# Kernel optimization log

Measured on AMD Instinct MI355X. Metric: run time of the kernel, lower is better.

Reference implementation:

```python
import jax, jax.numpy as jnp
import numpy as np

CHUNK = 512
LR = 0.001  # fast-weight learning_rate


def setup_inputs() -> dict:
    key = jax.random.key(0)
    k1, k2, k3, k4 = jax.random.split(key, 4)
    B, S, H, F = 4, 4096, 1024, 4096
    x = jax.random.normal(k1, (B, S, H), dtype=jnp.float32)
    w0 = jax.random.normal(k2, (H, F), dtype=jnp.float32) * 0.02
    w1 = jax.random.normal(k3, (F, H), dtype=jnp.float32) * 0.02
    w2 = jax.random.normal(k4, (H, F), dtype=jnp.float32) * 0.02
    return {"x": x, "w0": w0, "w1": w1, "w2": w2}


def _fast_weight(xc, a0, a1, a2):
    # SwiGLU fast-weight MLP (LaCT-style): [B,C,H] -> [B,C,H]
    h = jax.nn.silu(jnp.einsum('bch,hf->bcf', xc, a0)) * jnp.einsum('bch,hf->bcf', xc, a2)
    return jnp.einsum('bcf,fh->bch', h, a1)


def reference(x, w0, w1, w2):
    B, S, H = x.shape
    nC = S // CHUNK
    # [nC, B, CHUNK, H] so scan iterates over chunks
    xc = x.reshape(B, nC, CHUNK, H).transpose(1, 0, 2, 3)

    def step(carry, x_chunk):
        a0, a1, a2, acc_loss = carry
        out = _fast_weight(x_chunk, a0, a1, a2)
        chunk_loss = jnp.mean((out - x_chunk) ** 2)
        decay = 1.0 - LR * chunk_loss  # per-chunk scalar weight decay
        return (a0 * decay, a1 * decay, a2 * decay, acc_loss + chunk_loss), out

    init = (w0, w1, w2, jnp.float32(0.0))
    (_, _, _, total_loss), outs = jax.lax.scan(step, init, xc)
    output = outs.transpose(1, 0, 2, 3).reshape(B, S, H)
    return output, total_loss / nC
```

## Files before the change

### kernel.cpp

```cpp
#include <hip/hip_runtime.h>

typedef float f32x4 __attribute__((ext_vector_type(4)));
typedef short bf16x8 __attribute__((ext_vector_type(8)));
typedef unsigned short u16;

#define B_SZ 4
#define S_SZ 4096
#define H_SZ 1024
#define F_SZ 4096
#define CHUNK_SZ 512
#define NCHUNK 8
#define MCH 2048
#define LRATE 0.001f
#define NSPLIT 4

__device__ __forceinline__ u16 f2bf(float f) {
  unsigned u = __float_as_uint(f);
  u += 0x7FFFu + ((u >> 16) & 1u);
  return (u16)(u >> 16);
}
__device__ __forceinline__ float bf2f(u16 u) {
  return __uint_as_float(((unsigned)u) << 16);
}

__device__ __forceinline__ void gload_lds16(const void* g, void* l) {
  __builtin_amdgcn_global_load_lds(
      (const __attribute__((address_space(1))) unsigned int*)g,
      (__attribute__((address_space(3))) unsigned int*)l, 16, 0, 0);
}


__global__ __launch_bounds__(256) void k_init(float* scal) {
  if (threadIdx.x == 0) { scal[0] = 1.f; scal[1] = 0.f; }
}

__global__ __launch_bounds__(256) void k_cvt_x(const float* __restrict__ x,
                                               u16* __restrict__ xb) {
  size_t i = ((size_t)blockIdx.x * 256 + threadIdx.x) * 8;
  float4 v0 = *(const float4*)(x + i);
  float4 v1 = *(const float4*)(x + i + 4);
  union { u16 u[8]; bf16x8 v; } o;
  o.u[0] = f2bf(v0.x); o.u[1] = f2bf(v0.y); o.u[2] = f2bf(v0.z); o.u[3] = f2bf(v0.w);
  o.u[4] = f2bf(v1.x); o.u[5] = f2bf(v1.y); o.u[6] = f2bf(v1.z); o.u[7] = f2bf(v1.w);
  *(bf16x8*)(xb + i) = o.v;
}

__global__ __launch_bounds__(256) void k_transpose_cvt(const float* __restrict__ W,
                                                       u16* __restrict__ Wt,
                                                       int R, int C) {
  __shared__ float tile[32][33];
  int tx = threadIdx.x & 31, ty = threadIdx.x >> 5;
  int r0 = blockIdx.y << 5, c0 = blockIdx.x << 5;
#pragma unroll
  for (int i = 0; i < 4; i++)
    tile[ty + i * 8][tx] = W[(size_t)(r0 + ty + i * 8) * C + c0 + tx];
  __syncthreads();
#pragma unroll
  for (int i = 0; i < 4; i++)
    Wt[(size_t)(c0 + ty + i * 8) * R + r0 + tx] = f2bf(tile[tx][ty + i * 8]);
}

__global__ __launch_bounds__(256) void k_gemm_gu(
    const u16* __restrict__ xb,
    const u16* __restrict__ w0t,
    const u16* __restrict__ w2t,
    u16* __restrict__ hbuf,
    const float* __restrict__ scal, int chunk) {
  __shared__ __align__(16) u16 sA[128 * 64];
  __shared__ __align__(16) u16 sB0[64 * 64];
  __shared__ __align__(16) u16 sB2[64 * 64];

  int t = threadIdx.x;
  int lane = t & 63, wid = t >> 6;
  int wm = wid >> 1, wn = wid & 1;
  int tm = blockIdx.x, tn = blockIdx.y;

  int gm0 = tm << 7;
  int bb = gm0 >> 9;
  int pos0 = gm0 & 511;
  const u16* Abase = xb + ((size_t)bb * S_SZ + (size_t)chunk * CHUNK_SZ + pos0) * H_SZ;

  int srow = t >> 3;
  int scol = (((t & 7) ^ (srow & 7)) << 3);
  const u16* aSrc  = Abase + (size_t)srow * H_SZ + scol;
  const u16* b0Src = w0t + ((size_t)(tn << 6) + srow) * H_SZ + scol;
  const u16* b2Src = w2t + ((size_t)(tn << 6) + srow) * H_SZ + scol;
  char* aDst  = (char*)sA  + t * 16;
  char* b0Dst = (char*)sB0 + t * 16;
  char* b2Dst = (char*)sB2 + t * 16;

  f32x4 acc0[4][2], acc2[4][2];
#pragma unroll
  for (int i = 0; i < 4; i++)
#pragma unroll
    for (int j = 0; j < 2; j++)
#pragma unroll
      for (int k = 0; k < 4; k++) { acc0[i][j][k] = 0.f; acc2[i][j][k] = 0.f; }

  int arow = (wm << 6) + (lane & 15);
  int brow = (wn << 5) + (lane & 15);
  int sl0 = (lane >> 4) ^ (lane & 7);
  int sl1 = ((lane >> 4) | 4) ^ (lane & 7);
  const char* aP0 = (const char*)sA + arow * 128 + sl0 * 16;
  const char* aP1 = (const char*)sA + arow * 128 + sl1 * 16;
  const char* b0P0 = (const char*)sB0 + brow * 128 + sl0 * 16;
  const char* b0P1 = (const char*)sB0 + brow * 128 + sl1 * 16;
  const char* b2P0 = (const char*)sB2 + brow * 128 + sl0 * 16;
  const char* b2P1 = (const char*)sB2 + brow * 128 + sl1 * 16;

  for (int k0 = 0; k0 < H_SZ; k0 += 64) {
#pragma unroll
    for (int r = 0; r < 4; r++)
      gload_lds16(aSrc + (size_t)r * 32 * H_SZ, aDst + r * 4096);
#pragma unroll
    for (int r = 0; r < 2; r++) {
      gload_lds16(b0Src + (size_t)r * 32 * H_SZ, b0Dst + r * 4096);
      gload_lds16(b2Src + (size_t)r * 32 * H_SZ, b2Dst + r * 4096);
    }
    aSrc += 64; b0Src += 64; b2Src += 64;
    __syncthreads();

    {
      bf16x8 av[4], b0v[2], b2v[2];
#pragma unroll
      for (int fr = 0; fr < 4; fr++) av[fr] = *(const bf16x8*)(aP0 + fr * 2048);
#pragma unroll
      for (int fc = 0; fc < 2; fc++) {
        b0v[fc] = *(const bf16x8*)(b0P0 + fc * 2048);
        b2v[fc] = *(const bf16x8*)(b2P0 + fc * 2048);
      }
#pragma unroll
      for (int fr = 0; fr < 4; fr++)
#pragma unroll
        for (int fc = 0; fc < 2; fc++) {
          acc0[fr][fc] = __builtin_amdgcn_mfma_f32_16x16x32_bf16(av[fr], b0v[fc], acc0[fr][fc], 0, 0, 0);
          acc2[fr][fc] = __builtin_amdgcn_mfma_f32_16x16x32_bf16(av[fr], b2v[fc], acc2[fr][fc], 0, 0, 0);
        }
    }
    {
      bf16x8 av[4], b0v[2], b2v[2];
#pragma unroll
      for (int fr = 0; fr < 4; fr++) av[fr] = *(const bf16x8*)(aP1 + fr * 2048);
#pragma unroll
      for (int fc = 0; fc < 2; fc++) {
        b0v[fc] = *(const bf16x8*)(b0P1 + fc * 2048);
        b2v[fc] = *(const bf16x8*)(b2P1 + fc * 2048);
      }
#pragma unroll
      for (int fr = 0; fr < 4; fr++)
#pragma unroll
        for (int fc = 0; fc < 2; fc++) {
          acc0[fr][fc] = __builtin_amdgcn_mfma_f32_16x16x32_bf16(av[fr], b0v[fc], acc0[fr][fc], 0, 0, 0);
          acc2[fr][fc] = __builtin_amdgcn_mfma_f32_16x16x32_bf16(av[fr], b2v[fc], acc2[fr][fc], 0, 0, 0);
        }
    }
    __syncthreads();
  }

  float D = scal[0];
#pragma unroll
  for (int fr = 0; fr < 4; fr++)
#pragma unroll
    for (int fc = 0; fc < 2; fc++) {
      int row0 = (tm << 7) + (wm << 6) + (fr << 4) + ((lane >> 4) << 2);
      int col = (tn << 6) + (wn << 5) + (fc << 4) + (lane & 15);
#pragma unroll
      for (int j = 0; j < 4; j++) {
        float g = D * acc0[fr][fc][j];
        float u = D * acc2[fr][fc][j];
        float sil = g / (1.f + __expf(-g));
        hbuf[(size_t)(row0 + j) * F_SZ + col] = f2bf(sil * u);
      }
    }
}

__global__ __launch_bounds__(256) void k_gemm_out(
    const u16* __restrict__ hbuf,
    const u16* __restrict__ w1t,
    u16* __restrict__ pbuf) {
  __shared__ __align__(16) u16 sA[128 * 64];
  __shared__ __align__(16) u16 sB[64 * 64];

  int t = threadIdx.x;
  int lane = t & 63, wid = t >> 6;
  int wm = wid >> 1, wn = wid & 1;
  int tm = blockIdx.x, tn = blockIdx.y, kz = blockIdx.z;

  int srow = t >> 3;
  int scol = (((t & 7) ^ (srow & 7)) << 3);
  const u16* aSrc = hbuf + ((size_t)(tm << 7) + srow) * F_SZ + kz * 1024 + scol;
  const u16* bSrc = w1t + ((size_t)(tn << 6) + srow) * F_SZ + kz * 1024 + scol;
  char* aDst = (char*)sA + t * 16;
  char* bDst = (char*)sB + t * 16;

  f32x4 acc[4][2];
#pragma unroll
  for (int i = 0; i < 4; i++)
#pragma unroll
    for (int j = 0; j < 2; j++)
#pragma unroll
      for (int k = 0; k < 4; k++) acc[i][j][k] = 0.f;

  int arow = (wm << 6) + (lane & 15);
  int brow = (wn << 5) + (lane & 15);
  int sl0 = (lane >> 4) ^ (lane & 7);
  int sl1 = ((lane >> 4) | 4) ^ (lane & 7);
  const char* aP0 = (const char*)sA + arow * 128 + sl0 * 16;
  const char* aP1 = (const char*)sA + arow * 128 + sl1 * 16;
  const char* bP0 = (const char*)sB + brow * 128 + sl0 * 16;
  const char* bP1 = (const char*)sB + brow * 128 + sl1 * 16;

  for (int k0 = 0; k0 < 1024; k0 += 64) {
#pragma unroll
    for (int r = 0; r < 4; r++)
      gload_lds16(aSrc + (size_t)r * 32 * F_SZ, aDst + r * 4096);
#pragma unroll
    for (int r = 0; r < 2; r++)
      gload_lds16(bSrc + (size_t)r * 32 * F_SZ, bDst + r * 4096);
    aSrc += 64; bSrc += 64;
    __syncthreads();

    {
      bf16x8 av[4], bv[2];
#pragma unroll
      for (int fr = 0; fr < 4; fr++) av[fr] = *(const bf16x8*)(aP0 + fr * 2048);
#pragma unroll
      for (int fc = 0; fc < 2; fc++) bv[fc] = *(const bf16x8*)(bP0 + fc * 2048);
#pragma unroll
      for (int fr = 0; fr < 4; fr++)
#pragma unroll
        for (int fc = 0; fc < 2; fc++)
          acc[fr][fc] = __builtin_amdgcn_mfma_f32_16x16x32_bf16(av[fr], bv[fc], acc[fr][fc], 0, 0, 0);
    }
    {
      bf16x8 av[4], bv[2];
#pragma unroll
      for (int fr = 0; fr < 4; fr++) av[fr] = *(const bf16x8*)(aP1 + fr * 2048);
#pragma unroll
      for (int fc = 0; fc < 2; fc++) bv[fc] = *(const bf16x8*)(bP1 + fc * 2048);
#pragma unroll
      for (int fr = 0; fr < 4; fr++)
#pragma unroll
        for (int fc = 0; fc < 2; fc++)
          acc[fr][fc] = __builtin_amdgcn_mfma_f32_16x16x32_bf16(av[fr], bv[fc], acc[fr][fc], 0, 0, 0);
    }
    __syncthreads();
  }

#pragma unroll
  for (int fr = 0; fr < 4; fr++)
#pragma unroll
    for (int fc = 0; fc < 2; fc++) {
      int row0 = (tm << 7) + (wm << 6) + (fr << 4) + ((lane >> 4) << 2);
      int col = (tn << 6) + (wn << 5) + (fc << 4) + (lane & 15);
#pragma unroll
      for (int j = 0; j < 4; j++)
        pbuf[((size_t)kz * MCH + row0 + j) * 1024 + col] = f2bf(acc[fr][fc][j]);
    }
}

__global__ __launch_bounds__(256) void k_epilogue(
    const u16* __restrict__ pbuf, const float* __restrict__ x,
    float* __restrict__ out, const float* __restrict__ scal,
    float* __restrict__ partials, int chunk) {
  __shared__ float red[256];
  int t = threadIdx.x;
  size_t base = ((size_t)blockIdx.x * 256 + t) * 8;
  int row = (int)(base >> 10);
  int col = (int)(base & 1023);
  float D = scal[0];

  float s[8] = {0.f, 0.f, 0.f, 0.f, 0.f, 0.f, 0.f, 0.f};
#pragma unroll
  for (int kz = 0; kz < NSPLIT; kz++) {
    union { bf16x8 v; u16 u[8]; } p;
    p.v = *(const bf16x8*)(pbuf + (size_t)kz * MCH * 1024 + base);
#pragma unroll
    for (int j = 0; j < 8; j++) s[j] += bf2f(p.u[j]);
  }

  int bb = row >> 9, pos = row & 511;
  size_t off = ((size_t)bb * S_SZ + (size_t)chunk * CHUNK_SZ + pos) * H_SZ + col;
  float4 x0 = *(const float4*)(x + off);
  float4 x1 = *(const float4*)(x + off + 4);
  float xv[8] = {x0.x, x0.y, x0.z, x0.w, x1.x, x1.y, x1.z, x1.w};
  float ov[8];
  float psum = 0.f;
#pragma unroll
  for (int j = 0; j < 8; j++) {
    ov[j] = D * s[j];
    float e = ov[j] - xv[j];
    psum += e * e;
  }
  *(float4*)(out + off) = make_float4(ov[0], ov[1], ov[2], ov[3]);
  *(float4*)(out + off + 4) = make_float4(ov[4], ov[5], ov[6], ov[7]);

  red[t] = psum;
  __syncthreads();
  for (int s2 = 128; s2 > 0; s2 >>= 1) {
    if (t < s2) red[t] += red[t + s2];
    __syncthreads();
  }
  if (t == 0) partials[blockIdx.x] = red[0];
}

__global__ __launch_bounds__(256) void k_update(float* scal, const float* __restrict__ partials,
                                                float* lossout, int chunk) {
  __shared__ float red[256];
  int t = threadIdx.x;
  float s = 0.f;
  for (int i = t; i < 1024; i += 256) s += partials[i];
  red[t] = s;
  __syncthreads();
  for (int s2 = 128; s2 > 0; s2 >>= 1) {
    if (t < s2) red[t] += red[t + s2];
    __syncthreads();
  }
  if (t == 0) {
    float loss = red[0] / (float)((size_t)MCH * H_SZ);
    float total = scal[1] + loss;
    scal[1] = total;
    scal[0] = scal[0] * (1.f - LRATE * loss);
    if (chunk == NCHUNK - 1) lossout[0] = total / (float)NCHUNK;
  }
}

extern "C" void kernel_launch(void* const* d_in, const int* in_sizes, int n_in,
                              void* d_out, int out_size, void* d_ws, size_t ws_size,
                              hipStream_t stream) {
  const float* x = (const float*)d_in[0];
  const float* w0 = (const float*)d_in[1];
  const float* w1 = (const float*)d_in[2];
  const float* w2 = (const float*)d_in[3];
  float* out = (float*)d_out;

  char* ws = (char*)d_ws;
  float* scal = (float*)ws;
  float* partials = (float*)(ws + 1024);
  u16* xb = (u16*)(ws + 8192);
  u16* w0t = xb + (size_t)B_SZ * S_SZ * H_SZ;
  u16* w2t = w0t + (size_t)H_SZ * F_SZ;
  u16* w1t = w2t + (size_t)H_SZ * F_SZ;
  u16* hbuf = w1t + (size_t)F_SZ * H_SZ;
  u16* pbuf = hbuf + (size_t)MCH * F_SZ;

  k_init<<<1, 256, 0, stream>>>(scal);
  k_cvt_x<<<(B_SZ * S_SZ * H_SZ) / (256 * 8), 256, 0, stream>>>(x, xb);
  k_transpose_cvt<<<dim3(F_SZ / 32, H_SZ / 32), 256, 0, stream>>>(w0, w0t, H_SZ, F_SZ);
  k_transpose_cvt<<<dim3(H_SZ / 32, F_SZ / 32), 256, 0, stream>>>(w1, w1t, F_SZ, H_SZ);
  k_transpose_cvt<<<dim3(F_SZ / 32, H_SZ / 32), 256, 0, stream>>>(w2, w2t, H_SZ, F_SZ);

  float* lossout = out + (size_t)B_SZ * S_SZ * H_SZ;
  for (int c = 0; c < NCHUNK; c++) {
    k_gemm_gu<<<dim3(16, 64), 256, 0, stream>>>(xb, w0t, w2t, hbuf, scal, c);
    k_gemm_out<<<dim3(16, 16, NSPLIT), 256, 0, stream>>>(hbuf, w1t, pbuf);
    k_epilogue<<<1024, 256, 0, stream>>>(pbuf, x, out, scal, partials, c);
    k_update<<<1, 256, 0, stream>>>(scal, partials, lossout, c);
  }
}
```

Measured before the change: 627.4 us.

## Double-buffer LDS tiles and remap workgroups across XCDs in both GEMMs

Both GEMM kernels now keep two LDS buffers and issue the global-to-LDS loads for the next K step before computing on the current one. This lets memory latency overlap with MFMA work. The workgroup index is also permuted so consecutive blocks land on the same XCD, aiming for better L2 reuse of shared A/B tiles. LDS use doubles, which may lower occupancy, and with a single barrier per iteration the prefetch into the other buffer relies on the previous end-of-loop sync to stay safe.

Result: slower. 700.6 us (+11.7%).

```diff
diff --git a/kernel.cpp b/kernel.cpp
--- a/kernel.cpp
+++ b/kernel.cpp
@@ -66,14 +66,18 @@
     const u16* __restrict__ w2t,
     u16* __restrict__ hbuf,
     const float* __restrict__ scal, int chunk) {
-  __shared__ __align__(16) u16 sA[128 * 64];
-  __shared__ __align__(16) u16 sB0[64 * 64];
-  __shared__ __align__(16) u16 sB2[64 * 64];
+  __shared__ __align__(16) u16 sA[2][128 * 64];
+  __shared__ __align__(16) u16 sB0[2][64 * 64];
+  __shared__ __align__(16) u16 sB2[2][64 * 64];
 
   int t = threadIdx.x;
   int lane = t & 63, wid = t >> 6;
   int wm = wid >> 1, wn = wid & 1;
-  int tm = blockIdx.x, tn = blockIdx.y;
+
+  int orig = blockIdx.x + (gridDim.x * blockIdx.y);
+  int nwg = gridDim.x * gridDim.y;
+  int wg = (orig & 7) * (nwg >> 3) + (orig >> 3);
+  int tm = wg & 15, tn = wg >> 4;
 
   int gm0 = tm << 7;
   int bb = gm0 >> 9;
@@ -101,33 +105,46 @@
   int brow = (wn << 5) + (lane & 15);
   int sl0 = (lane >> 4) ^ (lane & 7);
   int sl1 = ((lane >> 4) | 4) ^ (lane & 7);
-  const char* aP0 = (const char*)sA + arow * 128 + sl0 * 16;
-  const char* aP1 = (const char*)sA + arow * 128 + sl1 * 16;
-  const char* b0P0 = (const char*)sB0 + brow * 128 + sl0 * 16;
-  const char* b0P1 = (const char*)sB0 + brow * 128 + sl1 * 16;
-  const char* b2P0 = (const char*)sB2 + brow * 128 + sl0 * 16;
-  const char* b2P1 = (const char*)sB2 + brow * 128 + sl1 * 16;
-
-  for (int k0 = 0; k0 < H_SZ; k0 += 64) {
-#pragma unroll
-    for (int r = 0; r < 4; r++)
-      gload_lds16(aSrc + (size_t)r * 32 * H_SZ, aDst + r * 4096);
-#pragma unroll
-    for (int r = 0; r < 2; r++) {
-      gload_lds16(b0Src + (size_t)r * 32 * H_SZ, b0Dst + r * 4096);
-      gload_lds16(b2Src + (size_t)r * 32 * H_SZ, b2Dst + r * 4096);
-    }
-    aSrc += 64; b0Src += 64; b2Src += 64;
-    __syncthreads();
-
+  const int aO0 = arow * 128 + sl0 * 16, aO1 = arow * 128 + sl1 * 16;
+  const int bO0 = brow * 128 + sl0 * 16, bO1 = brow * 128 + sl1 * 16;
+
+#pragma unroll
+  for (int r = 0; r < 4; r++)
+    gload_lds16(aSrc + (size_t)r * 32 * H_SZ, aDst + r * 4096);
+#pragma unroll
+  for (int r = 0; r < 2; r++) {
+    gload_lds16(b0Src + (size_t)r * 32 * H_SZ, b0Dst + r * 4096);
+    gload_lds16(b2Src + (size_t)r * 32 * H_SZ, b2Dst + r * 4096);
+  }
+  aSrc += 64; b0Src += 64; b2Src += 64;
+  __syncthreads();
+
+  int cur = 0;
+#pragma unroll 1
+  for (int step = 0; step < H_SZ / 64; step++) {
+    int nxt = cur ^ 1;
+    if (step + 1 < H_SZ / 64) {
+#pragma unroll
+      for (int r = 0; r < 4; r++)
+        gload_lds16(aSrc + (size_t)r * 32 * H_SZ, aDst + nxt * 16384 + r * 4096);
+#pragma unroll
+      for (int r = 0; r < 2; r++) {
+        gload_lds16(b0Src + (size_t)r * 32 * H_SZ, b0Dst + nxt * 8192 + r * 4096);
+        gload_lds16(b2Src + (size_t)r * 32 * H_SZ, b2Dst + nxt * 8192 + r * 4096);
+      }
+      aSrc += 64; b0Src += 64; b2Src += 64;
+    }
+    const char* aB  = (const char*)sA  + cur * 16384;
+    const char* b0B = (const char*)sB0 + cur * 8192;
+    const char* b2B = (const char*)sB2 + cur * 8192;
     {
       bf16x8 av[4], b0v[2], b2v[2];
 #pragma unroll
-      for (int fr = 0; fr < 4; fr++) av[fr] = *(const bf16x8*)(aP0 + fr * 2048);
+      for (int fr = 0; fr < 4; fr++) av[fr] = *(const bf16x8*)(aB + aO0 + fr * 2048);
 #pragma unroll
       for (int fc = 0; fc < 2; fc++) {
-        b0v[fc] = *(const bf16x8*)(b0P0 + fc * 2048);
-        b2v[fc] = *(const bf16x8*)(b2P0 + fc * 2048);
+        b0v[fc] = *(const bf16x8*)(b0B + bO0 + fc * 2048);
+        b2v[fc] = *(const bf16x8*)(b2B + bO0 + fc * 2048);
       }
 #pragma unroll
       for (int fr = 0; fr < 4; fr++)
@@ -140,11 +157,11 @@
     {
       bf16x8 av[4], b0v[2], b2v[2];
 #pragma unroll
-      for (int fr = 0; fr < 4; fr++) av[fr] = *(const bf16x8*)(aP1 + fr * 2048);
+      for (int fr = 0; fr < 4; fr++) av[fr] = *(const bf16x8*)(aB + aO1 + fr * 2048);
 #pragma unroll
       for (int fc = 0; fc < 2; fc++) {
-        b0v[fc] = *(const bf16x8*)(b0P1 + fc * 2048);
-        b2v[fc] = *(const bf16x8*)(b2P1 + fc * 2048);
+        b0v[fc] = *(const bf16x8*)(b0B + bO1 + fc * 2048);
+        b2v[fc] = *(const bf16x8*)(b2B + bO1 + fc * 2048);
       }
 #pragma unroll
       for (int fr = 0; fr < 4; fr++)
@@ -155,6 +172,7 @@
         }
     }
     __syncthreads();
+    cur = nxt;
   }
 
   float D = scal[0];
@@ -178,13 +196,17 @@
     const u16* __restrict__ hbuf,
     const u16* __restrict__ w1t,
     u16* __restrict__ pbuf) {
-  __shared__ __align__(16) u16 sA[128 * 64];
-  __shared__ __align__(16) u16 sB[64 * 64];
+  __shared__ __align__(16) u16 sA[2][128 * 64];
+  __shared__ __align__(16) u16 sB[2][64 * 64];
 
   int t = threadIdx.x;
   int lane = t & 63, wid = t >> 6;
   int wm = wid >> 1, wn = wid & 1;
-  int tm = blockIdx.x, tn = blockIdx.y, kz = blockIdx.z;
+
+  int orig = blockIdx.x + gridDim.x * (blockIdx.y + gridDim.y * blockIdx.z);
+  int nwg = gridDim.x * gridDim.y * gridDim.z;
+  int wg = (orig & 7) * (nwg >> 3) + (orig >> 3);
+  int tm = wg & 15, tn = (wg >> 4) & 15, kz = wg >> 8;
 
   int srow = t >> 3;
   int scol = (((t & 7) ^ (srow & 7)) << 3);
@@ -205,27 +227,39 @@
   int brow = (wn << 5) + (lane & 15);
   int sl0 = (lane >> 4) ^ (lane & 7);
   int sl1 = ((lane >> 4) | 4) ^ (lane & 7);
-  const char* aP0 = (const char*)sA + arow * 128 + sl0 * 16;
-  const char* aP1 = (const char*)sA + arow * 128 + sl1 * 16;
-  const char* bP0 = (const char*)sB + brow * 128 + sl0 * 16;
-  const char* bP1 = (const char*)sB + brow * 128 + sl1 * 16;
-
-  for (int k0 = 0; k0 < 1024; k0 += 64) {
-#pragma unroll
-    for (int r = 0; r < 4; r++)
-      gload_lds16(aSrc + (size_t)r * 32 * F_SZ, aDst + r * 4096);
-#pragma unroll
-    for (int r = 0; r < 2; r++)
-      gload_lds16(bSrc + (size_t)r * 32 * F_SZ, bDst + r * 4096);
-    aSrc += 64; bSrc += 64;
-    __syncthreads();
-
+  const int aO0 = arow * 128 + sl0 * 16, aO1 = arow * 128 + sl1 * 16;
+  const int bO0 = brow * 128 + sl0 * 16, bO1 = brow * 128 + sl1 * 16;
+
+#pragma unroll
+  for (int r = 0; r < 4; r++)
+    gload_lds16(aSrc + (size_t)r * 32 * F_SZ, aDst + r * 4096);
+#pragma unroll
+  for (int r = 0; r < 2; r++)
+    gload_lds16(bSrc + (size_t)r * 32 * F_SZ, bDst + r * 4096);
+  aSrc += 64; bSrc += 64;
+  __syncthreads();
+
+  int cur = 0;
+#pragma unroll 1
+  for (int step = 0; step < 1024 / 64; step++) {
+    int nxt = cur ^ 1;
+    if (step + 1 < 1024 / 64) {
+#pragma unroll
+      for (int r = 0; r < 4; r++)
+        gload_lds16(aSrc + (size_t)r * 32 * F_SZ, aDst + nxt * 16384 + r * 4096);
+#pragma unroll
+      for (int r = 0; r < 2; r++)
+        gload_lds16(bSrc + (size_t)r * 32 * F_SZ, bDst + nxt * 8192 + r * 4096);
+      aSrc += 64; bSrc += 64;
+    }
+    const char* aB = (const char*)sA + cur * 16384;
+    const char* bB = (const char*)sB + cur * 8192;
     {
       bf16x8 av[4], bv[2];
 #pragma unroll
-      for (int fr = 0; fr < 4; fr++) av[fr] = *(const bf16x8*)(aP0 + fr * 2048);
-#pragma unroll
-      for (int fc = 0; fc < 2; fc++) bv[fc] = *(const bf16x8*)(bP0 + fc * 2048);
+      for (int fr = 0; fr < 4; fr++) av[fr] = *(const bf16x8*)(aB + aO0 + fr * 2048);
+#pragma unroll
+      for (int fc = 0; fc < 2; fc++) bv[fc] = *(const bf16x8*)(bB + bO0 + fc * 2048);
 #pragma unroll
       for (int fr = 0; fr < 4; fr++)
 #pragma unroll
@@ -235,9 +269,9 @@
     {
       bf16x8 av[4], bv[2];
 #pragma unroll
-      for (int fr = 0; fr < 4; fr++) av[fr] = *(const bf16x8*)(aP1 + fr * 2048);
-#pragma unroll
-      for (int fc = 0; fc < 2; fc++) bv[fc] = *(const bf16x8*)(bP1 + fc * 2048);
+      for (int fr = 0; fr < 4; fr++) av[fr] = *(const bf16x8*)(aB + aO1 + fr * 2048);
+#pragma unroll
+      for (int fc = 0; fc < 2; fc++) bv[fc] = *(const bf16x8*)(bB + bO1 + fc * 2048);
 #pragma unroll
       for (int fr = 0; fr < 4; fr++)
 #pragma unroll
@@ -245,6 +279,7 @@
           acc[fr][fc] = __builtin_amdgcn_mfma_f32_16x16x32_bf16(av[fr], bv[fc], acc[fr][fc], 0, 0, 0);
     }
     __syncthreads();
+    cur = nxt;
   }
 
 #pragma unroll
```

## Double-buffer LDS tiles with BK=32 and remap workgroups for XCD locality

Applied to the files above, without the earlier changes.

Both GEMM kernels now use two LDS buffers holding 32-wide K slices instead of one 64-wide slice, so the async global-to-LDS load of the next slice is issued before computing the current one, overlapping memory with MFMA work. The LDS swizzle is reworked for the 64-byte row stride. The gate/up kernel also remaps block IDs round-robin across 8 groups, presumably to match the XCDs and improve L2 reuse of shared weight tiles. The cost is twice as many barriers per K, and the remap hardcodes tm = wg & 15, which assumes a grid of 16 row tiles.

New measurement: 764.0 us. 21.8% more time.

```diff
diff --git a/kernel.cpp b/kernel.cpp
--- a/kernel.cpp
+++ b/kernel.cpp
@@ -66,28 +66,29 @@
     const u16* __restrict__ w2t,
     u16* __restrict__ hbuf,
     const float* __restrict__ scal, int chunk) {
-  __shared__ __align__(16) u16 sA[128 * 64];
-  __shared__ __align__(16) u16 sB0[64 * 64];
-  __shared__ __align__(16) u16 sB2[64 * 64];
+  __shared__ __align__(16) u16 sA[2][128 * 32];
+  __shared__ __align__(16) u16 sB0[2][64 * 32];
+  __shared__ __align__(16) u16 sB2[2][64 * 32];
 
   int t = threadIdx.x;
   int lane = t & 63, wid = t >> 6;
   int wm = wid >> 1, wn = wid & 1;
-  int tm = blockIdx.x, tn = blockIdx.y;
+
+  int orig = blockIdx.x + (gridDim.x * blockIdx.y);
+  int nwg = gridDim.x * gridDim.y;
+  int wg = (orig & 7) * (nwg >> 3) + (orig >> 3);
+  int tm = wg & 15, tn = wg >> 4;
 
   int gm0 = tm << 7;
   int bb = gm0 >> 9;
   int pos0 = gm0 & 511;
   const u16* Abase = xb + ((size_t)bb * S_SZ + (size_t)chunk * CHUNK_SZ + pos0) * H_SZ;
 
-  int srow = t >> 3;
-  int scol = (((t & 7) ^ (srow & 7)) << 3);
+  int srow = t >> 2;
+  int scol = (((t & 3) ^ ((srow >> 1) & 3)) << 3);
   const u16* aSrc  = Abase + (size_t)srow * H_SZ + scol;
   const u16* b0Src = w0t + ((size_t)(tn << 6) + srow) * H_SZ + scol;
   const u16* b2Src = w2t + ((size_t)(tn << 6) + srow) * H_SZ + scol;
-  char* aDst  = (char*)sA  + t * 16;
-  char* b0Dst = (char*)sB0 + t * 16;
-  char* b2Dst = (char*)sB2 + t * 16;
 
   f32x4 acc0[4][2], acc2[4][2];
 #pragma unroll
@@ -97,63 +98,51 @@
 #pragma unroll
       for (int k = 0; k < 4; k++) { acc0[i][j][k] = 0.f; acc2[i][j][k] = 0.f; }
 
-  int arow = (wm << 6) + (lane & 15);
-  int brow = (wn << 5) + (lane & 15);
-  int sl0 = (lane >> 4) ^ (lane & 7);
-  int sl1 = ((lane >> 4) | 4) ^ (lane & 7);
-  const char* aP0 = (const char*)sA + arow * 128 + sl0 * 16;
-  const char* aP1 = (const char*)sA + arow * 128 + sl1 * 16;
-  const char* b0P0 = (const char*)sB0 + brow * 128 + sl0 * 16;
-  const char* b0P1 = (const char*)sB0 + brow * 128 + sl1 * 16;
-  const char* b2P0 = (const char*)sB2 + brow * 128 + sl0 * 16;
-  const char* b2P1 = (const char*)sB2 + brow * 128 + sl1 * 16;
-
-  for (int k0 = 0; k0 < H_SZ; k0 += 64) {
-#pragma unroll
-    for (int r = 0; r < 4; r++)
-      gload_lds16(aSrc + (size_t)r * 32 * H_SZ, aDst + r * 4096);
-#pragma unroll
-    for (int r = 0; r < 2; r++) {
-      gload_lds16(b0Src + (size_t)r * 32 * H_SZ, b0Dst + r * 4096);
-      gload_lds16(b2Src + (size_t)r * 32 * H_SZ, b2Dst + r * 4096);
-    }
-    aSrc += 64; b0Src += 64; b2Src += 64;
-    __syncthreads();
-
-    {
-      bf16x8 av[4], b0v[2], b2v[2];
-#pragma unroll
-      for (int fr = 0; fr < 4; fr++) av[fr] = *(const bf16x8*)(aP0 + fr * 2048);
-#pragma unroll
-      for (int fc = 0; fc < 2; fc++) {
-        b0v[fc] = *(const bf16x8*)(b0P0 + fc * 2048);
-        b2v[fc] = *(const bf16x8*)(b2P0 + fc * 2048);
-      }
-#pragma unroll
-      for (int fr = 0; fr < 4; fr++)
-#pragma unroll
-        for (int fc = 0; fc < 2; fc++) {
-          acc0[fr][fc] = __builtin_amdgcn_mfma_f32_16x16x32_bf16(av[fr], b0v[fc], acc0[fr][fc], 0, 0, 0);
-          acc2[fr][fc] = __builtin_amdgcn_mfma_f32_16x16x32_bf16(av[fr], b2v[fc], acc2[fr][fc], 0, 0, 0);
-        }
-    }
-    {
-      bf16x8 av[4], b0v[2], b2v[2];
-#pragma unroll
-      for (int fr = 0; fr < 4; fr++) av[fr] = *(const bf16x8*)(aP1 + fr * 2048);
-#pragma unroll
-      for (int fc = 0; fc < 2; fc++) {
-        b0v[fc] = *(const bf16x8*)(b0P1 + fc * 2048);
-        b2v[fc] = *(const bf16x8*)(b2P1 + fc * 2048);
-      }
-#pragma unroll
-      for (int fr = 0; fr < 4; fr++)
-#pragma unroll
-        for (int fc = 0; fc < 2; fc++) {
-          acc0[fr][fc] = __builtin_amdgcn_mfma_f32_16x16x32_bf16(av[fr], b0v[fc], acc0[fr][fc], 0, 0, 0);
-          acc2[fr][fc] = __builtin_amdgcn_mfma_f32_16x16x32_bf16(av[fr], b2v[fc], acc2[fr][fc], 0, 0, 0);
-        }
-    }
+  int rsl = (lane >> 4) ^ (((lane & 15) >> 1) & 3);
+  const int aO = ((wm << 6) + (lane & 15)) * 64 + rsl * 16;
+  const int bO = ((wn << 5) + (lane & 15)) * 64 + rsl * 16;
+
+#define GU_PREFETCH(b)                                                     \
+  {                                                                        \
+    gload_lds16(aSrc, (char*)sA + (b)*8192 + t * 16);                      \
+    gload_lds16(aSrc + (size_t)64 * H_SZ, (char*)sA + (b)*8192 + 4096 + t * 16); \
+    gload_lds16(b0Src, (char*)sB0 + (b)*4096 + t * 16);                    \
+    gload_lds16(b2Src, (char*)sB2 + (b)*4096 + t * 16);                    \
+    aSrc += 32; b0Src += 32; b2Src += 32;                                  \
+  }
+
+#define GU_COMPUTE(b)                                                      \
+  {                                                                        \
+    const char* aB  = (const char*)sA  + (b)*8192;                         \
+    const char* b0B = (const char*)sB0 + (b)*4096;                         \
+    const char* b2B = (const char*)sB2 + (b)*4096;                         \
+    bf16x8 av[4], b0v[2], b2v[2];                                          \
+    _Pragma("unroll")                                                      \
+    for (int fr = 0; fr < 4; fr++) av[fr] = *(const bf16x8*)(aB + aO + fr * 1024); \
+    _Pragma("unroll")                                                      \
+    for (int fc = 0; fc < 2; fc++) {                                       \
+      b0v[fc] = *(const bf16x8*)(b0B + bO + fc * 1024);                    \
+      b2v[fc] = *(const bf16x8*)(b2B + bO + fc * 1024);                    \
+    }                                                                      \
+    _Pragma("unroll")                                                      \
+    for (int fr = 0; fr < 4; fr++)                                         \
+      _Pragma("unroll")                                                    \
+      for (int fc = 0; fc < 2; fc++) {                                     \
+        acc0[fr][fc] = __builtin_amdgcn_mfma_f32_16x16x32_bf16(av[fr], b0v[fc], acc0[fr][fc], 0, 0, 0); \
+        acc2[fr][fc] = __builtin_amdgcn_mfma_f32_16x16x32_bf16(av[fr], b2v[fc], acc2[fr][fc], 0, 0, 0); \
+      }                                                                    \
+  }
+
+  GU_PREFETCH(0);
+  __syncthreads();
+
+#pragma unroll 1
+  for (int step = 0; step < 32; step += 2) {
+    if (step + 1 < 32) GU_PREFETCH(1);
+    GU_COMPUTE(0);
+    __syncthreads();
+    if (step + 2 < 32) GU_PREFETCH(0);
+    GU_COMPUTE(1);
     __syncthreads();
   }
 
@@ -178,20 +167,18 @@
     const u16* __restrict__ hbuf,
     const u16* __restrict__ w1t,
     u16* __restrict__ pbuf) {
-  __shared__ __align__(16) u16 sA[128 * 64];
-  __shared__ __align__(16) u16 sB[64 * 64];
+  __shared__ __align__(16) u16 sA[2][128 * 32];
+  __shared__ __align__(16) u16 sB[2][64 * 32];
 
   int t = threadIdx.x;
   int lane = t & 63, wid = t >> 6;
   int wm = wid >> 1, wn = wid & 1;
   int tm = blockIdx.x, tn = blockIdx.y, kz = blockIdx.z;
 
-  int srow = t >> 3;
-  int scol = (((t & 7) ^ (srow & 7)) << 3);
+  int srow = t >> 2;
+  int scol = (((t & 3) ^ ((srow >> 1) & 3)) << 3);
   const u16* aSrc = hbuf + ((size_t)(tm << 7) + srow) * F_SZ + kz * 1024 + scol;
   const u16* bSrc = w1t + ((size_t)(tn << 6) + srow) * F_SZ + kz * 1024 + scol;
-  char* aDst = (char*)sA + t * 16;
-  char* bDst = (char*)sB + t * 16;
 
   f32x4 acc[4][2];
 #pragma unroll
@@ -201,49 +188,44 @@
 #pragma unroll
       for (int k = 0; k < 4; k++) acc[i][j][k] = 0.f;
 
-  int arow = (wm << 6) + (lane & 15);
-  int brow = (wn << 5) + (lane & 15);
-  int sl0 = (lane >> 4) ^ (lane & 7);
-  int sl1 = ((lane >> 4) | 4) ^ (lane & 7);
-  const char* aP0 = (const char*)sA + arow * 128 + sl0 * 16;
-  const char* aP1 = (const char*)sA + arow * 128 + sl1 * 16;
-  const char* bP0 = (const char*)sB + brow * 128 + sl0 * 16;
-  const char* bP1 = (const char*)sB + brow * 128 + sl1 * 16;
-
-  for (int k0 = 0; k0 < 1024; k0 += 64) {
-#pragma unroll
-    for (int r = 0; r < 4; r++)
-      gload_lds16(aSrc + (size_t)r * 32 * F_SZ, aDst + r * 4096);
-#pragma unroll
-    for (int r = 0; r < 2; r++)
-      gload_lds16(bSrc + (size_t)r * 32 * F_SZ, bDst + r * 4096);
-    aSrc += 64; bSrc += 64;
-    __syncthreads();
-
-    {
-      bf16x8 av[4], bv[2];
-#pragma unroll
-      for (int fr = 0; fr < 4; fr++) av[fr] = *(const bf16x8*)(aP0 + fr * 2048);
-#pragma unroll
-      for (int fc = 0; fc < 2; fc++) bv[fc] = *(const bf16x8*)(bP0 + fc * 2048);
-#pragma unroll
-      for (int fr = 0; fr < 4; fr++)
-#pragma unroll
-        for (int fc = 0; fc < 2; fc++)
-          acc[fr][fc] = __builtin_amdgcn_mfma_f32_16x16x32_bf16(av[fr], bv[fc], acc[fr][fc], 0, 0, 0);
-    }
-    {
-      bf16x8 av[4], bv[2];
-#pragma unroll
-      for (int fr = 0; fr < 4; fr++) av[fr] = *(const bf16x8*)(aP1 + fr * 2048);
-#pragma unroll
-      for (int fc = 0; fc < 2; fc++) bv[fc] = *(const bf16x8*)(bP1 + fc * 2048);
-#pragma unroll
-      for (int fr = 0; fr < 4; fr++)
-#pragma unroll
-        for (int fc = 0; fc < 2; fc++)
-          acc[fr][fc] = __builtin_amdgcn_mfma_f32_16x16x32_bf16(av[fr], bv[fc], acc[fr][fc], 0, 0, 0);
-    }
+  int rsl = (lane >> 4) ^ (((lane & 15) >> 1) & 3);
+  const int aO = ((wm << 6) + (lane & 15)) * 64 + rsl * 16;
+  const int bO = ((wn << 5) + (lane & 15)) * 64 + rsl * 16;
+
+#define GO_PREFETCH(b)                                                     \
+  {                                                                        \
+    gload_lds16(aSrc, (char*)sA + (b)*8192 + t * 16);                      \
+    gload_lds16(aSrc + (size_t)64 * F_SZ, (char*)sA + (b)*8192 + 4096 + t * 16); \
+    gload_lds16(bSrc, (char*)sB + (b)*4096 + t * 16);                      \
+    aSrc += 32; bSrc += 32;                                                \
+  }
+
+#define GO_COMPUTE(b)                                                      \
+  {                                                                        \
+    const char* aB = (const char*)sA + (b)*8192;                           \
+    const char* bB = (const char*)sB + (b)*4096;                           \
+    bf16x8 av[4], bv[2];                                                   \
+    _Pragma("unroll")                                                      \
+    for (int fr = 0; fr < 4; fr++) av[fr] = *(const bf16x8*)(aB + aO + fr * 1024); \
+    _Pragma("unroll")                                                      \
+    for (int fc = 0; fc < 2; fc++) bv[fc] = *(const bf16x8*)(bB + bO + fc * 1024); \
+    _Pragma("unroll")                                                      \
+    for (int fr = 0; fr < 4; fr++)                                         \
+      _Pragma("unroll")                                                    \
+      for (int fc = 0; fc < 2; fc++)                                       \
+        acc[fr][fc] = __builtin_amdgcn_mfma_f32_16x16x32_bf16(av[fr], bv[fc], acc[fr][fc], 0, 0, 0); \
+  }
+
+  GO_PREFETCH(0);
+  __syncthreads();
+
+#pragma unroll 1
+  for (int step = 0; step < 32; step += 2) {
+    if (step + 1 < 32) GO_PREFETCH(1);
+    GO_COMPUTE(0);
+    __syncthreads();
+    if (step + 2 < 32) GO_PREFETCH(0);
+    GO_COMPUTE(1);
     __syncthreads();
   }
 
```

## Widen gate/up GEMM tile to 128x128 with XCD-aware block remapping

Applied to the files above, without the earlier changes.

The gate/up GEMM tile grows from 128x64 to 128x128 columns per block, with each wave computing a 64x64 sub-tile (4x4 MFMA fragments per weight). This halves the grid and the re-reads of the x tile from global memory. A block-index swizzle groups consecutive work-groups by XCD so that neighbouring tiles share L2. The cost is doubled accumulator registers (128 fp32 per weight matrix) and more LDS, with launch_bounds(256,2) pinning occupancy at a risk of spills. LDS reads now use integer offsets, and the K loops are kept rolled.

Measured after the change: 606.4 us. 1.03x faster.

```diff
diff --git a/kernel.cpp b/kernel.cpp
--- a/kernel.cpp
+++ b/kernel.cpp
@@ -60,20 +60,24 @@
     Wt[(size_t)(c0 + ty + i * 8) * R + r0 + tx] = f2bf(tile[tx][ty + i * 8]);
 }
 
-__global__ __launch_bounds__(256) void k_gemm_gu(
+__global__ __launch_bounds__(256, 2) void k_gemm_gu(
     const u16* __restrict__ xb,
     const u16* __restrict__ w0t,
     const u16* __restrict__ w2t,
     u16* __restrict__ hbuf,
     const float* __restrict__ scal, int chunk) {
   __shared__ __align__(16) u16 sA[128 * 64];
-  __shared__ __align__(16) u16 sB0[64 * 64];
-  __shared__ __align__(16) u16 sB2[64 * 64];
+  __shared__ __align__(16) u16 sB0[128 * 64];
+  __shared__ __align__(16) u16 sB2[128 * 64];
 
   int t = threadIdx.x;
   int lane = t & 63, wid = t >> 6;
   int wm = wid >> 1, wn = wid & 1;
-  int tm = blockIdx.x, tn = blockIdx.y;
+
+  int orig = blockIdx.x + (gridDim.x * blockIdx.y);
+  int nwg = gridDim.x * gridDim.y;
+  int wg = (orig & 7) * (nwg >> 3) + (orig >> 3);
+  int tm = wg & 15, tn = wg >> 4;
 
   int gm0 = tm << 7;
   int bb = gm0 >> 9;
@@ -83,37 +87,32 @@
   int srow = t >> 3;
   int scol = (((t & 7) ^ (srow & 7)) << 3);
   const u16* aSrc  = Abase + (size_t)srow * H_SZ + scol;
-  const u16* b0Src = w0t + ((size_t)(tn << 6) + srow) * H_SZ + scol;
-  const u16* b2Src = w2t + ((size_t)(tn << 6) + srow) * H_SZ + scol;
+  const u16* b0Src = w0t + ((size_t)(tn << 7) + srow) * H_SZ + scol;
+  const u16* b2Src = w2t + ((size_t)(tn << 7) + srow) * H_SZ + scol;
   char* aDst  = (char*)sA  + t * 16;
   char* b0Dst = (char*)sB0 + t * 16;
   char* b2Dst = (char*)sB2 + t * 16;
 
-  f32x4 acc0[4][2], acc2[4][2];
+  f32x4 acc0[4][4], acc2[4][4];
 #pragma unroll
   for (int i = 0; i < 4; i++)
 #pragma unroll
-    for (int j = 0; j < 2; j++)
+    for (int j = 0; j < 4; j++)
 #pragma unroll
       for (int k = 0; k < 4; k++) { acc0[i][j][k] = 0.f; acc2[i][j][k] = 0.f; }
 
   int arow = (wm << 6) + (lane & 15);
-  int brow = (wn << 5) + (lane & 15);
+  int brow = (wn << 6) + (lane & 15);
   int sl0 = (lane >> 4) ^ (lane & 7);
   int sl1 = ((lane >> 4) | 4) ^ (lane & 7);
-  const char* aP0 = (const char*)sA + arow * 128 + sl0 * 16;
-  const char* aP1 = (const char*)sA + arow * 128 + sl1 * 16;
-  const char* b0P0 = (const char*)sB0 + brow * 128 + sl0 * 16;
-  const char* b0P1 = (const char*)sB0 + brow * 128 + sl1 * 16;
-  const char* b2P0 = (const char*)sB2 + brow * 128 + sl0 * 16;
-  const char* b2P1 = (const char*)sB2 + brow * 128 + sl1 * 16;
-
+  const int aO0 = arow * 128 + sl0 * 16, aO1 = arow * 128 + sl1 * 16;
+  const int bO0 = brow * 128 + sl0 * 16, bO1 = brow * 128 + sl1 * 16;
+
+#pragma unroll 1
   for (int k0 = 0; k0 < H_SZ; k0 += 64) {
 #pragma unroll
-    for (int r = 0; r < 4; r++)
-      gload_lds16(aSrc + (size_t)r * 32 * H_SZ, aDst + r * 4096);
-#pragma unroll
-    for (int r = 0; r < 2; r++) {
+    for (int r = 0; r < 4; r++) {
+      gload_lds16(aSrc  + (size_t)r * 32 * H_SZ, aDst  + r * 4096);
       gload_lds16(b0Src + (size_t)r * 32 * H_SZ, b0Dst + r * 4096);
       gload_lds16(b2Src + (size_t)r * 32 * H_SZ, b2Dst + r * 4096);
     }
@@ -121,35 +120,35 @@
     __syncthreads();
 
     {
-      bf16x8 av[4], b0v[2], b2v[2];
-#pragma unroll
-      for (int fr = 0; fr < 4; fr++) av[fr] = *(const bf16x8*)(aP0 + fr * 2048);
-#pragma unroll
-      for (int fc = 0; fc < 2; fc++) {
-        b0v[fc] = *(const bf16x8*)(b0P0 + fc * 2048);
-        b2v[fc] = *(const bf16x8*)(b2P0 + fc * 2048);
+      bf16x8 av[4], b0v[4], b2v[4];
+#pragma unroll
+      for (int fr = 0; fr < 4; fr++) av[fr] = *(const bf16x8*)((const char*)sA + aO0 + fr * 2048);
+#pragma unroll
+      for (int fc = 0; fc < 4; fc++) {
+        b0v[fc] = *(const bf16x8*)((const char*)sB0 + bO0 + fc * 2048);
+        b2v[fc] = *(const bf16x8*)((const char*)sB2 + bO0 + fc * 2048);
       }
 #pragma unroll
       for (int fr = 0; fr < 4; fr++)
 #pragma unroll
-        for (int fc = 0; fc < 2; fc++) {
+        for (int fc = 0; fc < 4; fc++) {
           acc0[fr][fc] = __builtin_amdgcn_mfma_f32_16x16x32_bf16(av[fr], b0v[fc], acc0[fr][fc], 0, 0, 0);
           acc2[fr][fc] = __builtin_amdgcn_mfma_f32_16x16x32_bf16(av[fr], b2v[fc], acc2[fr][fc], 0, 0, 0);
         }
     }
     {
-      bf16x8 av[4], b0v[2], b2v[2];
-#pragma unroll
-      for (int fr = 0; fr < 4; fr++) av[fr] = *(const bf16x8*)(aP1 + fr * 2048);
-#pragma unroll
-      for (int fc = 0; fc < 2; fc++) {
-        b0v[fc] = *(const bf16x8*)(b0P1 + fc * 2048);
-        b2v[fc] = *(const bf16x8*)(b2P1 + fc * 2048);
+      bf16x8 av[4], b0v[4], b2v[4];
+#pragma unroll
+      for (int fr = 0; fr < 4; fr++) av[fr] = *(const bf16x8*)((const char*)sA + aO1 + fr * 2048);
+#pragma unroll
+      for (int fc = 0; fc < 4; fc++) {
+        b0v[fc] = *(const bf16x8*)((const char*)sB0 + bO1 + fc * 2048);
+        b2v[fc] = *(const bf16x8*)((const char*)sB2 + bO1 + fc * 2048);
       }
 #pragma unroll
       for (int fr = 0; fr < 4; fr++)
 #pragma unroll
-        for (int fc = 0; fc < 2; fc++) {
+        for (int fc = 0; fc < 4; fc++) {
           acc0[fr][fc] = __builtin_amdgcn_mfma_f32_16x16x32_bf16(av[fr], b0v[fc], acc0[fr][fc], 0, 0, 0);
           acc2[fr][fc] = __builtin_amdgcn_mfma_f32_16x16x32_bf16(av[fr], b2v[fc], acc2[fr][fc], 0, 0, 0);
         }
@@ -161,9 +160,9 @@
 #pragma unroll
   for (int fr = 0; fr < 4; fr++)
 #pragma unroll
-    for (int fc = 0; fc < 2; fc++) {
+    for (int fc = 0; fc < 4; fc++) {
       int row0 = (tm << 7) + (wm << 6) + (fr << 4) + ((lane >> 4) << 2);
-      int col = (tn << 6) + (wn << 5) + (fc << 4) + (lane & 15);
+      int col = (tn << 7) + (wn << 6) + (fc << 4) + (lane & 15);
 #pragma unroll
       for (int j = 0; j < 4; j++) {
         float g = D * acc0[fr][fc][j];
@@ -205,11 +204,10 @@
   int brow = (wn << 5) + (lane & 15);
   int sl0 = (lane >> 4) ^ (lane & 7);
   int sl1 = ((lane >> 4) | 4) ^ (lane & 7);
-  const char* aP0 = (const char*)sA + arow * 128 + sl0 * 16;
-  const char* aP1 = (const char*)sA + arow * 128 + sl1 * 16;
-  const char* bP0 = (const char*)sB + brow * 128 + sl0 * 16;
-  const char* bP1 = (const char*)sB + brow * 128 + sl1 * 16;
-
+  const int aO0 = arow * 128 + sl0 * 16, aO1 = arow * 128 + sl1 * 16;
+  const int bO0 = brow * 128 + sl0 * 16, bO1 = brow * 128 + sl1 * 16;
+
+#pragma unroll 1
   for (int k0 = 0; k0 < 1024; k0 += 64) {
 #pragma unroll
     for (int r = 0; r < 4; r++)
@@ -223,9 +221,9 @@
     {
       bf16x8 av[4], bv[2];
 #pragma unroll
-      for (int fr = 0; fr < 4; fr++) av[fr] = *(const bf16x8*)(aP0 + fr * 2048);
-#pragma unroll
-      for (int fc = 0; fc < 2; fc++) bv[fc] = *(const bf16x8*)(bP0 + fc * 2048);
+      for (int fr = 0; fr < 4; fr++) av[fr] = *(const bf16x8*)((const char*)sA + aO0 + fr * 2048);
+#pragma unroll
+      for (int fc = 0; fc < 2; fc++) bv[fc] = *(const bf16x8*)((const char*)sB + bO0 + fc * 2048);
 #pragma unroll
       for (int fr = 0; fr < 4; fr++)
 #pragma unroll
@@ -235,9 +233,9 @@
     {
       bf16x8 av[4], bv[2];
 #pragma unroll
-      for (int fr = 0; fr < 4; fr++) av[fr] = *(const bf16x8*)(aP1 + fr * 2048);
-#pragma unroll
-      for (int fc = 0; fc < 2; fc++) bv[fc] = *(const bf16x8*)(bP1 + fc * 2048);
+      for (int fr = 0; fr < 4; fr++) av[fr] = *(const bf16x8*)((const char*)sA + aO1 + fr * 2048);
+#pragma unroll
+      for (int fc = 0; fc < 2; fc++) bv[fc] = *(const bf16x8*)((const char*)sB + bO1 + fc * 2048);
 #pragma unroll
       for (int fr = 0; fr < 4; fr++)
 #pragma unroll
@@ -352,7 +350,7 @@
 
   float* lossout = out + (size_t)B_SZ * S_SZ * H_SZ;
   for (int c = 0; c < NCHUNK; c++) {
-    k_gemm_gu<<<dim3(16, 64), 256, 0, stream>>>(xb, w0t, w2t, hbuf, scal, c);
+    k_gemm_gu<<<dim3(16, 32), 256, 0, stream>>>(xb, w0t, w2t, hbuf, scal, c);
     k_gemm_out<<<dim3(16, 16, NSPLIT), 256, 0, stream>>>(hbuf, w1t, pbuf);
     k_epilogue<<<1024, 256, 0, stream>>>(pbuf, x, out, scal, partials, c);
     k_update<<<1, 256, 0, stream>>>(scal, partials, lossout, c);
```
